# Performance work log

Hardware: AMD Instinct MI355X
Metric: run time of the kernel (lower is better)

Reference implementation:

```python
import jax, jax.numpy as jnp
import numpy as np

N = 20000       # nodes
E = 320000      # edges (before self-loops)
F_IN = 1024     # num_features
H = 4           # head_num
C = 64          # hidden_size
NC = 4          # n_classes
NEG_SLOPE = 0.2 # PyG GATConv default


def setup_inputs() -> dict:
    key = jax.random.key(0)
    ks = jax.random.split(key, 16)
    def w(k, shape, fan_in):
        return jax.random.normal(k, shape, dtype=jnp.float32) / np.sqrt(fan_in)
    x = jax.random.normal(ks[0], (N, F_IN), dtype=jnp.float32)
    edge_index = jax.random.randint(ks[1], (2, E), 0, N, dtype=jnp.int64)
    return {
        "x": x,
        "edge_index": edge_index,
        # layer 1: F_IN -> H*C, concat
        "w1": w(ks[2], (F_IN, H * C), F_IN),
        "as1": w(ks[3], (H, C), C),
        "ad1": w(ks[4], (H, C), C),
        "b1": jnp.zeros((H * C,), jnp.float32),
        # layer 2: H*C -> H*C, concat
        "w2": w(ks[5], (H * C, H * C), H * C),
        "as2": w(ks[6], (H, C), C),
        "ad2": w(ks[7], (H, C), C),
        "b2": jnp.zeros((H * C,), jnp.float32),
        # out layer: H*C -> C, 1 head, concat=False
        "w3": w(ks[8], (H * C, 1 * C), H * C),
        "as3": w(ks[9], (1, C), C),
        "ad3": w(ks[10], (1, C), C),
        "b3": jnp.zeros((C,), jnp.float32),
        # classifier
        "wc": w(ks[11], (C, NC), C),
        "bc": jnp.zeros((NC,), jnp.float32),
    }


def gat_layer(x, src, dst, W, a_src, a_dst, bias, concat):
    """PyG GATConv (eval mode, self-loops already added to src/dst)."""
    n = x.shape[0]
    Hh, Cc = a_src.shape
    h = (x @ W).reshape(n, Hh, Cc)                       # [N,H,C]
    al_s = jnp.sum(h * a_src[None], axis=-1)             # [N,H]
    al_d = jnp.sum(h * a_dst[None], axis=-1)             # [N,H]
    e = al_s[src] + al_d[dst]                            # [E,H]
    e = jax.nn.leaky_relu(e, NEG_SLOPE)
    # segment softmax over incoming edges of each destination node
    emax = jax.ops.segment_max(e, dst, num_segments=n)   # [N,H]
    ex = jnp.exp(e - emax[dst])
    denom = jax.ops.segment_sum(ex, dst, num_segments=n) # [N,H]
    alpha = ex / (denom[dst] + 1e-16)                    # [E,H]
    msg = h[src] * alpha[..., None]                      # [E,H,C]
    out = jax.ops.segment_sum(msg, dst, num_segments=n)  # [N,H,C]
    if concat:
        out = out.reshape(n, Hh * Cc)
    else:
        out = out.mean(axis=1)
    return out + bias


def reference(x, edge_index, w1, as1, ad1, b1, w2, as2, ad2, b2,
              w3, as3, ad3, b3, wc, bc):
    n = x.shape[0]
    loop = jnp.arange(n, dtype=edge_index.dtype)
    src = jnp.concatenate([edge_index[0], loop])
    dst = jnp.concatenate([edge_index[1], loop])
    out = jax.nn.relu(gat_layer(x, src, dst, w1, as1, ad1, b1, True))
    out = jax.nn.relu(gat_layer(out, src, dst, w2, as2, ad2, b2, True))
    out = gat_layer(out, src, dst, w3, as3, ad3, b3, False)
    return out @ wc + bc                                  # [N, n_classes]
```

## Files before the change

kernel.cpp:

```cpp
#include <hip/hip_runtime.h>

#define N_NODES 20000
#define N_EDGES 320000
#define ET (N_EDGES + N_NODES)
#define F_IN 1024
#define HC 256
#define NC 4

typedef unsigned short ushort_t;
typedef __attribute__((ext_vector_type(8))) short short8;
typedef __attribute__((ext_vector_type(4))) float f32x4;

__device__ inline ushort_t f2bf(float f) {
    unsigned u = __float_as_uint(f);
    unsigned r = (u + 0x7fffu + ((u >> 16) & 1u)) >> 16;
    return (ushort_t)r;
}
__device__ inline float bf2f(ushort_t u) {
    return __uint_as_float(((unsigned)u) << 16);
}

__device__ inline unsigned cvt_pk_bf16(float lo, float hi) {
    unsigned r;
    asm("v_cvt_pk_bf16_f32 %0, %1, %2" : "=v"(r) : "v"(lo), "v"(hi));
    return r;
}

#define GLOAD16(gp, lp) __builtin_amdgcn_global_load_lds( \
    (const __attribute__((address_space(1))) void*)(gp),  \
    (__attribute__((address_space(3))) void*)(lp), 16, 0, 0)

__global__ void prep_kernel(const int* __restrict__ ei, int* __restrict__ counts,
                            const float* __restrict__ w1, ushort_t* __restrict__ w1Th,
                            ushort_t* __restrict__ w1Tl,
                            const float* __restrict__ w2, ushort_t* __restrict__ w2Th,
                            ushort_t* __restrict__ w2Tl,
                            const float* __restrict__ w3, ushort_t* __restrict__ w3Th,
                            ushort_t* __restrict__ w3Tl) {
    const int EB = (ET + 255) / 256;
    const int S1 = F_IN * HC / 256;
    const int S2 = HC * HC / 256;
    int b = blockIdx.x;
    if (b < EB) {
        int e = b * 256 + threadIdx.x;
        if (e < ET) {
            int dst = (e < N_EDGES) ? ei[N_EDGES + e] : (e - N_EDGES);
            atomicAdd(&counts[dst], 1);
        }
    } else if (b < EB + S1) {
        int idx = (b - EB) * 256 + threadIdx.x;
        int k = idx / HC, n = idx - k * HC;
        float v = w1[idx];
        ushort_t h = f2bf(v);
        w1Th[(size_t)n * F_IN + k] = h;
        w1Tl[(size_t)n * F_IN + k] = f2bf(v - bf2f(h));
    } else if (b < EB + S1 + S2) {
        int idx = (b - EB - S1) * 256 + threadIdx.x;
        int k = idx / HC, n = idx - k * HC;
        float v = w2[idx];
        ushort_t h = f2bf(v);
        w2Th[(size_t)n * HC + k] = h;
        w2Tl[(size_t)n * HC + k] = f2bf(v - bf2f(h));
    } else {
        int idx = (b - EB - S1 - S2) * 256 + threadIdx.x;
        int k = idx / 64, n = idx - k * 64;
        float v = w3[idx];
        ushort_t h = f2bf(v);
        w3Th[(size_t)n * HC + k] = h;
        w3Tl[(size_t)n * HC + k] = f2bf(v - bf2f(h));
    }
}

__global__ void scan_kernel(const int* __restrict__ counts, int* __restrict__ row_ptr,
                            int* __restrict__ cursor) {
    __shared__ int sums[1024];
    int t = threadIdx.x;
    const int per = (N_NODES + 1023) / 1024;
    int b = t * per;
    int e = min(b + per, N_NODES);
    int s = 0;
    for (int i = b; i < e; ++i) s += counts[i];
    sums[t] = s;
    __syncthreads();
    for (int off = 1; off < 1024; off <<= 1) {
        int v = (t >= off) ? sums[t - off] : 0;
        __syncthreads();
        sums[t] += v;
        __syncthreads();
    }
    int run = (t == 0) ? 0 : sums[t - 1];
    for (int i = b; i < e; ++i) {
        row_ptr[i] = run;
        cursor[i]  = run;
        run += counts[i];
    }
    if (t == 0) row_ptr[N_NODES] = ET;
}

__global__ void scatter_kernel(const int* __restrict__ ei, int* __restrict__ cursor,
                               int* __restrict__ col) {
    int e = blockIdx.x * blockDim.x + threadIdx.x;
    if (e >= ET) return;
    int src, dst;
    if (e < N_EDGES) { src = ei[e]; dst = ei[N_EDGES + e]; }
    else             { src = dst = e - N_EDGES; }
    int pos = atomicAdd(&cursor[dst], 1);
    col[pos] = src;
}

#define AL_EPILOGUE()                                                              \
    {                                                                              \
        float asv[NF], adv[NF];                                                    \
        _Pragma("unroll")                                                          \
        for (int j = 0; j < NF; ++j) {                                             \
            int col = bn + wn * SN + j * 16 + (lane & 15);                         \
            asv[j] = as_w[col];                                                    \
            adv[j] = ad_w[col];                                                    \
        }                                                                          \
        float* s_as = (float*)smem;                                   \
        float* s_ad = (float*)smem + 2 * BM;                                       \
        _Pragma("unroll")                                                          \
        for (int i = 0; i < MF; ++i) {                                             \
            _Pragma("unroll")                                                      \
            for (int rr = 0; rr < 4; ++rr) {                                       \
                float ps = 0.f, pd = 0.f;                                          \
                _Pragma("unroll")                                                  \
                for (int j = 0; j < NF; ++j) {                                     \
                    ps += acc[i][j][rr] * asv[j];                                  \
                    pd += acc[i][j][rr] * adv[j];                                  \
                }                                                                  \
                _Pragma("unroll")                                                  \
                for (int o = 1; o < 16; o <<= 1) {                                 \
                    ps += __shfl_xor(ps, o, 64);                                   \
                    pd += __shfl_xor(pd, o, 64);                                   \
                }                                                                  \
                if ((lane & 15) == 0) {                                            \
                    int rl = wm * SM + i * 16 + (lane >> 4) * 4 + rr;              \
                    s_as[wn * BM + rl] = ps;                                       \
                    s_ad[wn * BM + rl] = pd;                                       \
                }                                                                  \
            }                                                                      \
        }                                                                          \
        __syncthreads();                                                           \
        if (t < BM) {                                                              \
            int row = bm + t;                                                      \
            if (row < M) {                                                         \
                int hb = bn >> 6;                                                  \
                als[row * H + hb] = s_as[t] + s_as[BM + t];                        \
                ald[row * H + hb] = s_ad[t] + s_ad[BM + t];                        \
            }                                                                      \
        }                                                                          \
    }

template<int GY>
__launch_bounds__(256)
__global__ void gemm_f32a_ks(const float* __restrict__ X,
                             const ushort_t* __restrict__ BTh, const ushort_t* __restrict__ BTl,
                             float* __restrict__ Cp0, float* __restrict__ Cp1,
                             int M, int K, int NT) {
    constexpr int BM = 128, BN = 64, SM = 64, SN = 32, MF = 4, NF = 2;
    __shared__ __align__(16) char smem[49152];

    const int t = threadIdx.x, lane = t & 63, w = t >> 6;
    const int wm = w >> 1, wn = w & 1;
    const int nwg = gridDim.x;
    const int id = blockIdx.x;
    const int q = nwg >> 3, r = nwg & 7;
    const int xcd = id & 7, idx = id >> 3;
    const int logical = (xcd < r ? xcd * (q + 1) : r * (q + 1) + (xcd - r) * q) + idx;
    const int nwg_half = nwg >> 1;
    const int ks = logical / nwg_half;
    const int rem = logical - ks * nwg_half;
    const int bm = (rem / GY) * BM, bn = (rem % GY) * BN;
    const int kbase = ks * (K >> 1);
    float* Cp = ks ? Cp1 : Cp0;

    size_t gA[4]; int lA[4];
    #pragma unroll
    for (int qq = 0; qq < 4; ++qq) {
        int row  = (w * 4 + qq) * 8 + (lane >> 3);
        int grow = min(bm + row, M - 1);
        int sw16 = ((((lane >> 1) & 3) ^ (row & 3)) << 1) | (lane & 1);
        gA[qq] = ((size_t)grow * K + kbase) * 4 + sw16 * 16;
        lA[qq] = (w * 4 + qq) * 1024;
    }
    const int gchunk = ((lane & 3) ^ ((lane >> 3) & 3)) * 16;
    const int brow = w * 16 + (lane >> 2);
    const size_t gB = (size_t)(bn + brow) * K * 2 + (size_t)kbase * 2 + gchunk;
    const int lB = w * 1024;

    const char* Xb  = (const char*)X;
    const char* Bhb = (const char*)BTh;
    const char* Blb = (const char*)BTl;
    const int c16 = (lane >> 4);
    const int NTs = K >> 7;

    f32x4 acc[MF][NF];
    #pragma unroll
    for (int i = 0; i < MF; ++i)
        #pragma unroll
        for (int j = 0; j < NF; ++j) acc[i][j] = (f32x4){0.f, 0.f, 0.f, 0.f};

    for (int ts = 0; ts < NTs; ++ts) {
        size_t kbB = (size_t)ts * 128;
        size_t kbA = (size_t)ts * 256;
        #pragma unroll
        for (int kc = 0; kc < 2; ++kc) {
            #pragma unroll
            for (int qq = 0; qq < 4; ++qq)
                GLOAD16(Xb + gA[qq] + kbA + kc * 128, smem + kc * 16384 + lA[qq]);
            GLOAD16(Bhb + gB + kbB + kc * 64, smem + 32768 + kc * 4096 + lB);
            GLOAD16(Blb + gB + kbB + kc * 64, smem + 40960 + kc * 4096 + lB);
        }
        __syncthreads();
        #pragma unroll
        for (int kc = 0; kc < 2; ++kc) {
            short8 afh[MF], afl[MF], bfh[NF], bfl[NF];
            #pragma unroll
            for (int i = 0; i < MF; ++i) {
                int row = wm * SM + i * 16 + (lane & 15);
                int off = kc * 16384 + row * 128 + ((c16 ^ (row & 3)) * 32);
                float4 a0 = *(const float4*)(smem + off);
                float4 a1 = *(const float4*)(smem + off + 16);
                unsigned h0 = cvt_pk_bf16(a0.x, a0.y);
                unsigned h1 = cvt_pk_bf16(a0.z, a0.w);
                unsigned h2 = cvt_pk_bf16(a1.x, a1.y);
                unsigned h3 = cvt_pk_bf16(a1.z, a1.w);
                unsigned l0 = cvt_pk_bf16(a0.x - __uint_as_float(h0 << 16),
                                          a0.y - __uint_as_float(h0 & 0xFFFF0000u));
                unsigned l1 = cvt_pk_bf16(a0.z - __uint_as_float(h1 << 16),
                                          a0.w - __uint_as_float(h1 & 0xFFFF0000u));
                unsigned l2 = cvt_pk_bf16(a1.x - __uint_as_float(h2 << 16),
                                          a1.y - __uint_as_float(h2 & 0xFFFF0000u));
                unsigned l3 = cvt_pk_bf16(a1.z - __uint_as_float(h3 << 16),
                                          a1.w - __uint_as_float(h3 & 0xFFFF0000u));
                uint4 hv = make_uint4(h0, h1, h2, h3);
                uint4 lv = make_uint4(l0, l1, l2, l3);
                afh[i] = *(short8*)&hv;
                afl[i] = *(short8*)&lv;
            }
            #pragma unroll
            for (int j = 0; j < NF; ++j) {
                int row = wn * SN + j * 16 + (lane & 15);
                int off = row * 64 + ((c16 ^ ((row >> 1) & 3)) * 16);
                bfh[j] = *(const short8*)(smem + 32768 + kc * 4096 + off);
                bfl[j] = *(const short8*)(smem + 40960 + kc * 4096 + off);
            }
            #pragma unroll
            for (int i = 0; i < MF; ++i)
                #pragma unroll
                for (int j = 0; j < NF; ++j) {
                    acc[i][j] = __builtin_amdgcn_mfma_f32_16x16x32_bf16(afh[i], bfh[j], acc[i][j], 0, 0, 0);
                    acc[i][j] = __builtin_amdgcn_mfma_f32_16x16x32_bf16(afh[i], bfl[j], acc[i][j], 0, 0, 0);
                    acc[i][j] = __builtin_amdgcn_mfma_f32_16x16x32_bf16(afl[i], bfh[j], acc[i][j], 0, 0, 0);
                }
        }
        __syncthreads();
    }
    #pragma unroll
    for (int i = 0; i < MF; ++i) {
        int rbase = bm + wm * SM + i * 16 + (lane >> 4) * 4;
        #pragma unroll
        for (int j = 0; j < NF; ++j) {
            int col = bn + wn * SN + j * 16 + (lane & 15);
            #pragma unroll
            for (int rr = 0; rr < 4; ++rr)
                if (rbase + rr < M) Cp[(size_t)(rbase + rr) * NT + col] = acc[i][j][rr];
        }
    }
}

__launch_bounds__(256)
__global__ void reduce_al(float* __restrict__ B0, const float* __restrict__ Cp1,
                          const float* __restrict__ as_w, const float* __restrict__ ad_w,
                          float* __restrict__ als, float* __restrict__ ald) {
    int lane = threadIdx.x & 63, w = threadIdx.x >> 6;
    int row = blockIdx.x * 4 + w;
    if (row >= N_NODES) return;
    size_t base = (size_t)row * HC + lane * 4;
    float4 p0 = *(const float4*)&B0[base];
    float4 p1 = *(const float4*)&Cp1[base];
    float4 s = make_float4(p0.x + p1.x, p0.y + p1.y, p0.z + p1.z, p0.w + p1.w);
    *(float4*)&B0[base] = s;
    int head = lane >> 4;
    int cw = (lane & 15) * 4;
    float ps = s.x * as_w[head * 64 + cw + 0] + s.y * as_w[head * 64 + cw + 1]
             + s.z * as_w[head * 64 + cw + 2] + s.w * as_w[head * 64 + cw + 3];
    float pd = s.x * ad_w[head * 64 + cw + 0] + s.y * ad_w[head * 64 + cw + 1]
             + s.z * ad_w[head * 64 + cw + 2] + s.w * ad_w[head * 64 + cw + 3];
    #pragma unroll
    for (int o = 1; o < 16; o <<= 1) {
        ps += __shfl_xor(ps, o, 64);
        pd += __shfl_xor(pd, o, 64);
    }
    if ((lane & 15) == 0) {
        als[row * 4 + head] = ps;
        ald[row * 4 + head] = pd;
    }
}

template<int BMT, int GY, int H>
__launch_bounds__(256)
__global__ void gemm_mfma(const ushort_t* __restrict__ Ah, const ushort_t* __restrict__ Al,
                          const ushort_t* __restrict__ BTh, const ushort_t* __restrict__ BTl,
                          float* __restrict__ C, const float* __restrict__ as_w,
                          const float* __restrict__ ad_w, float* __restrict__ als,
                          float* __restrict__ ald, int M, int K, int NT) {
    constexpr int BM = BMT, BN = 64, SM = BM / 2, SN = 32, MF = SM / 16, NF = 2;
    constexpr int AQ = BM / 64;
    constexpr int ASZ = BM * 64;
    __shared__ __align__(16) char smem[4 * ASZ + 16384];

    const int t = threadIdx.x, lane = t & 63, w = t >> 6;
    const int wm = w >> 1, wn = w & 1;
    const int nwg = gridDim.x;
    const int id = blockIdx.x;
    const int q = nwg >> 3, r = nwg & 7;
    const int xcd = id & 7, idx = id >> 3;
    const int logical = (xcd < r ? xcd * (q + 1) : r * (q + 1) + (xcd - r) * q) + idx;
    const int bm = (logical / GY) * BM, bn = (logical % GY) * BN;
    const int gchunk = ((lane & 3) ^ ((lane >> 3) & 3)) * 16;

    size_t gA[AQ]; int lA[AQ];
    #pragma unroll
    for (int qq = 0; qq < AQ; ++qq) {
        int inst = w * AQ + qq;
        int arow = inst * 16 + (lane >> 2);
        int grow = min(bm + arow, M - 1);
        gA[qq] = (size_t)grow * K * 2 + gchunk;
        lA[qq] = inst * 1024;
    }
    const int brow = w * 16 + (lane >> 2);
    const size_t gB = (size_t)(bn + brow) * K * 2 + gchunk;
    const int lB = w * 1024;

    const char* Ahb = (const char*)Ah;
    const char* Alb = (const char*)Al;
    const char* Bhb = (const char*)BTh;
    const char* Blb = (const char*)BTl;
    const int c16 = (lane >> 4);
    const int NTs = K / 64;

    f32x4 acc[MF][NF];
    #pragma unroll
    for (int i = 0; i < MF; ++i)
        #pragma unroll
        for (int j = 0; j < NF; ++j) acc[i][j] = (f32x4){0.f, 0.f, 0.f, 0.f};

    for (int ts = 0; ts < NTs; ++ts) {
        size_t kb = (size_t)ts * 128;
        #pragma unroll
        for (int kc = 0; kc < 2; ++kc) {
            #pragma unroll
            for (int qq = 0; qq < AQ; ++qq) {
                GLOAD16(Ahb + gA[qq] + kb + kc * 64, smem + kc * ASZ + lA[qq]);
                GLOAD16(Alb + gA[qq] + kb + kc * 64, smem + 2 * ASZ + kc * ASZ + lA[qq]);
            }
            GLOAD16(Bhb + gB + kb + kc * 64, smem + 4 * ASZ + kc * 4096 + lB);
            GLOAD16(Blb + gB + kb + kc * 64, smem + 4 * ASZ + 8192 + kc * 4096 + lB);
        }
        __syncthreads();
        #pragma unroll
        for (int kc = 0; kc < 2; ++kc) {
            short8 afh[MF], afl[MF], bfh[NF], bfl[NF];
            #pragma unroll
            for (int i = 0; i < MF; ++i) {
                int row = wm * SM + i * 16 + (lane & 15);
                int off = row * 64 + ((c16 ^ ((row >> 1) & 3)) * 16);
                afh[i] = *(const short8*)(smem + kc * ASZ + off);
                afl[i] = *(const short8*)(smem + 2 * ASZ + kc * ASZ + off);
            }
            #pragma unroll
            for (int j = 0; j < NF; ++j) {
                int row = wn * SN + j * 16 + (lane & 15);
                int off = row * 64 + ((c16 ^ ((row >> 1) & 3)) * 16);
                bfh[j] = *(const short8*)(smem + 4 * ASZ + kc * 4096 + off);
                bfl[j] = *(const short8*)(smem + 4 * ASZ + 8192 + kc * 4096 + off);
            }
            #pragma unroll
            for (int i = 0; i < MF; ++i)
                #pragma unroll
                for (int j = 0; j < NF; ++j) {
                    acc[i][j] = __builtin_amdgcn_mfma_f32_16x16x32_bf16(afh[i], bfh[j], acc[i][j], 0, 0, 0);
                    acc[i][j] = __builtin_amdgcn_mfma_f32_16x16x32_bf16(afh[i], bfl[j], acc[i][j], 0, 0, 0);
                    acc[i][j] = __builtin_amdgcn_mfma_f32_16x16x32_bf16(afl[i], bfh[j], acc[i][j], 0, 0, 0);
                }
        }
        __syncthreads();
    }
    #pragma unroll
    for (int i = 0; i < MF; ++i) {
        int rbase = bm + wm * SM + i * 16 + (lane >> 4) * 4;
        #pragma unroll
        for (int j = 0; j < NF; ++j) {
            int col = bn + wn * SN + j * 16 + (lane & 15);
            #pragma unroll
            for (int rr = 0; rr < 4; ++rr)
                if (rbase + rr < M) C[(size_t)(rbase + rr) * NT + col] = acc[i][j][rr];
        }
    }
    AL_EPILOGUE()
}

template<int CT, int CW, int H, bool RELU, bool SPLIT, bool CLS>
__launch_bounds__(256)
__global__ void agg_v6(const float* __restrict__ h, const float* __restrict__ als,
                       const float* __restrict__ ald,
                       const int* __restrict__ row_ptr, const int* __restrict__ col,
                       const float* __restrict__ bias,
                       ushort_t* __restrict__ oh, ushort_t* __restrict__ ol,
                       float* __restrict__ of,
                       const float* __restrict__ wc, const float* __restrict__ bc,
                       float* __restrict__ cls_out) {
    constexpr int NS  = CT / CW;
    constexpr int LPT = CW / 4;
    constexpr int TPW = 64 / LPT;
    static_assert(NS == H, "slice==head mapping");
    __shared__ int   s_src[4][64];
    __shared__ float s_alp[4][64];
    const int nwg = gridDim.x;
    const int q = nwg >> 3;
    int id = blockIdx.x;
    int logical = (id & 7) * q + (id >> 3);
    int slice = logical / (N_NODES / 4);
    int g = logical - slice * (N_NODES / 4);
    int lane = threadIdx.x & 63, w = threadIdx.x >> 6;
    int dst = g * 4 + w;
    int beg = row_ptr[dst], deg = row_ptr[dst + 1] - beg;
    int team = lane / LPT;
    int cc = (lane & (LPT - 1)) * 4;

    const int*   colP = col + beg;
    const float* hS   = h + slice * CW + cc;
    float ad = ald[dst * H + slice];

    float m = -1e30f, den = 0.f;
    for (int base = 0; base < deg; base += 64) {
        int i = base + lane;
        if (i < deg) {
            float e = als[colP[i] * H + slice] + ad;
            e = (e > 0.f) ? e : 0.2f * e;
            float nm = fmaxf(m, e);
            den = den * __expf(m - nm) + __expf(e - nm);
            m = nm;
        }
    }
    #pragma unroll
    for (int off = 1; off < 64; off <<= 1) {
        float mo = __shfl_xor(m, off, 64);
        float dn = __shfl_xor(den, off, 64);
        float nm = fmaxf(m, mo);
        den = den * __expf(m - nm) + dn * __expf(mo - nm);
        m = nm;
    }
    float rden = 1.f / (den + 1e-16f);

    float4 a0v = make_float4(0.f, 0.f, 0.f, 0.f);
    float4 a1v = make_float4(0.f, 0.f, 0.f, 0.f);
    float4 a2v = make_float4(0.f, 0.f, 0.f, 0.f);
    float4 a3v = make_float4(0.f, 0.f, 0.f, 0.f);
    for (int base = 0; base < deg; base += 64) {
        int cnt = min(64, deg - base);
        if (lane < cnt) {
            int src = colP[base + lane];
            s_src[w][lane] = src;
            float e = als[src * H + slice] + ad;
            e = (e > 0.f) ? e : 0.2f * e;
            s_alp[w][lane] = __expf(e - m) * rden;
        }
        int i = team;
        for (; i + 3 * TPW < cnt; i += 4 * TPW) {
            int   s0 = s_src[w][i],           s1 = s_src[w][i + TPW];
            int   s2 = s_src[w][i + 2 * TPW], s3 = s_src[w][i + 3 * TPW];
            float a0 = s_alp[w][i],           a1 = s_alp[w][i + TPW];
            float a2 = s_alp[w][i + 2 * TPW], a3 = s_alp[w][i + 3 * TPW];
            float4 h0 = *(const float4*)&hS[s0 * CT];
            float4 h1 = *(const float4*)&hS[s1 * CT];
            float4 h2 = *(const float4*)&hS[s2 * CT];
            float4 h3 = *(const float4*)&hS[s3 * CT];
            a0v.x += a0 * h0.x; a0v.y += a0 * h0.y; a0v.z += a0 * h0.z; a0v.w += a0 * h0.w;
            a1v.x += a1 * h1.x; a1v.y += a1 * h1.y; a1v.z += a1 * h1.z; a1v.w += a1 * h1.w;
            a2v.x += a2 * h2.x; a2v.y += a2 * h2.y; a2v.z += a2 * h2.z; a2v.w += a2 * h2.w;
            a3v.x += a3 * h3.x; a3v.y += a3 * h3.y; a3v.z += a3 * h3.z; a3v.w += a3 * h3.w;
        }
        for (; i < cnt; i += TPW) {
            int   s0 = s_src[w][i];
            float a0 = s_alp[w][i];
            float4 h0 = *(const float4*)&hS[s0 * CT];
            a0v.x += a0 * h0.x; a0v.y += a0 * h0.y; a0v.z += a0 * h0.z; a0v.w += a0 * h0.w;
        }
    }
    float4 acc = make_float4((a0v.x + a1v.x) + (a2v.x + a3v.x),
                             (a0v.y + a1v.y) + (a2v.y + a3v.y),
                             (a0v.z + a1v.z) + (a2v.z + a3v.z),
                             (a0v.w + a1v.w) + (a2v.w + a3v.w));
    #pragma unroll
    for (int off = LPT; off < 64; off <<= 1) {
        acc.x += __shfl_xor(acc.x, off, 64);
        acc.y += __shfl_xor(acc.y, off, 64);
        acc.z += __shfl_xor(acc.z, off, 64);
        acc.w += __shfl_xor(acc.w, off, 64);
    }
    if (team == 0) {
        int ch = slice * CW + cc;
        float4 bv = *(const float4*)&bias[ch];
        float v0 = acc.x + bv.x, v1 = acc.y + bv.y, v2 = acc.z + bv.z, v3 = acc.w + bv.w;
        if (RELU) {
            v0 = fmaxf(v0, 0.f); v1 = fmaxf(v1, 0.f);
            v2 = fmaxf(v2, 0.f); v3 = fmaxf(v3, 0.f);
        }
        if (CLS) {
            float ps[NC];
            #pragma unroll
            for (int k = 0; k < NC; ++k)
                ps[k] = v0 * wc[(cc + 0) * NC + k] + v1 * wc[(cc + 1) * NC + k]
                      + v2 * wc[(cc + 2) * NC + k] + v3 * wc[(cc + 3) * NC + k];
            #pragma unroll
            for (int o = 1; o < 16; o <<= 1)
                #pragma unroll
                for (int k = 0; k < NC; ++k) ps[k] += __shfl_xor(ps[k], o, 64);
            if (lane == 0) {
                #pragma unroll
                for (int k = 0; k < NC; ++k) cls_out[(size_t)dst * NC + k] = ps[k] + bc[k];
            }
        } else {
            size_t idx = (size_t)dst * CT + ch;
            if (SPLIT) {
                ushort4 h4, l4;
                h4.x = f2bf(v0); l4.x = f2bf(v0 - bf2f(h4.x));
                h4.y = f2bf(v1); l4.y = f2bf(v1 - bf2f(h4.y));
                h4.z = f2bf(v2); l4.z = f2bf(v2 - bf2f(h4.z));
                h4.w = f2bf(v3); l4.w = f2bf(v3 - bf2f(h4.w));
                *(ushort4*)&oh[idx] = h4;
                *(ushort4*)&ol[idx] = l4;
            } else {
                *(float4*)&of[idx] = make_float4(v0, v1, v2, v3);
            }
        }
    }
}

extern "C" void kernel_launch(void* const* d_in, const int* in_sizes, int n_in,
                              void* d_out, int out_size, void* d_ws, size_t ws_size,
                              hipStream_t stream) {
    const float* x   = (const float*)d_in[0];
    const int*   ei  = (const int*)d_in[1];
    const float* w1  = (const float*)d_in[2];
    const float* as1 = (const float*)d_in[3];
    const float* ad1 = (const float*)d_in[4];
    const float* b1  = (const float*)d_in[5];
    const float* w2  = (const float*)d_in[6];
    const float* as2 = (const float*)d_in[7];
    const float* ad2 = (const float*)d_in[8];
    const float* b2  = (const float*)d_in[9];
    const float* w3  = (const float*)d_in[10];
    const float* as3 = (const float*)d_in[11];
    const float* ad3 = (const float*)d_in[12];
    const float* b3  = (const float*)d_in[13];
    const float* wc  = (const float*)d_in[14];
    const float* bc  = (const float*)d_in[15];
    float* out = (float*)d_out;

    char* ws = (char*)d_ws;
    size_t off = 0;
    auto alloc = [&](size_t bytes) -> char* {
        char* p = ws + off;
        off = (off + bytes + 255) & ~(size_t)255;
        return p;
    };

    int* counts  = (int*)alloc(N_NODES * 4);
    int* cursor  = (int*)alloc(N_NODES * 4);
    int* row_ptr = (int*)alloc((N_NODES + 1) * 4);
    int* colidx  = (int*)alloc(ET * 4);
    float* als   = (float*)alloc(N_NODES * 4 * 4);
    float* ald   = (float*)alloc(N_NODES * 4 * 4);
    float* B0    = (float*)alloc((size_t)N_NODES * HC * 4);
    float* Cp1   = (float*)alloc((size_t)N_NODES * HC * 4);

    ushort_t* w1Th = (ushort_t*)alloc((size_t)F_IN * HC * 2);
    ushort_t* w1Tl = (ushort_t*)alloc((size_t)F_IN * HC * 2);
    ushort_t* w2Th = (ushort_t*)alloc((size_t)HC * HC * 2);
    ushort_t* w2Tl = (ushort_t*)alloc((size_t)HC * HC * 2);
    ushort_t* w3Th = (ushort_t*)alloc((size_t)HC * 64 * 2);
    ushort_t* w3Tl = (ushort_t*)alloc((size_t)HC * 64 * 2);
    ushort_t* B1h  = (ushort_t*)alloc((size_t)N_NODES * HC * 2);
    ushort_t* B1l  = (ushort_t*)alloc((size_t)N_NODES * HC * 2);

    hipMemsetAsync(counts, 0, N_NODES * sizeof(int), stream);
    const int EB = (ET + 255) / 256;
    const int PREP = EB + F_IN * HC / 256 + HC * HC / 256 + HC * 64 / 256;
    prep_kernel<<<PREP, 256, 0, stream>>>(ei, counts, w1, w1Th, w1Tl,
                                          w2, w2Th, w2Tl, w3, w3Th, w3Tl);
    scan_kernel<<<1, 1024, 0, stream>>>(counts, row_ptr, cursor);
    scatter_kernel<<<EB, 256, 0, stream>>>(ei, cursor, colidx);

    const int nwg128 = ((N_NODES + 127) / 128) * (HC / 64);
    const int nblk_dst = N_NODES / 4;
    gemm_f32a_ks<4><<<2 * nwg128, 256, 0, stream>>>(x, w1Th, w1Tl, B0, Cp1, N_NODES, F_IN, HC);
    reduce_al<<<nblk_dst, 256, 0, stream>>>(B0, Cp1, as1, ad1, als, ald);
    agg_v6<256, 64, 4, true, true, false><<<4 * nblk_dst, 256, 0, stream>>>(
        B0, als, ald, row_ptr, colidx, b1, B1h, B1l, nullptr, nullptr, nullptr, nullptr);
    gemm_mfma<128, 4, 4><<<nwg128, 256, 0, stream>>>(B1h, B1l, w2Th, w2Tl, B0, as2, ad2,
                                                     als, ald, N_NODES, HC, HC);
    agg_v6<256, 64, 4, true, true, false><<<4 * nblk_dst, 256, 0, stream>>>(
        B0, als, ald, row_ptr, colidx, b2, B1h, B1l, nullptr, nullptr, nullptr, nullptr);
    const int nwg3 = (N_NODES + 63) / 64;
    gemm_mfma<64, 1, 1><<<nwg3, 256, 0, stream>>>(B1h, B1l, w3Th, w3Tl, B0, as3, ad3,
                                                  als, ald, N_NODES, HC, 64);
    agg_v6<64, 64, 1, false, false, true><<<nblk_dst, 256, 0, stream>>>(
        B0, als, ald, row_ptr, colidx, b3, nullptr, nullptr, nullptr, wc, bc, out);
}
```

Before: 287.6 us.

## Load A operand directly from global into registers, bypassing LDS staging

The fp32 X tile is now read straight from global memory into registers, laid out to match the MFMA fragments, and no longer staged through shared memory with swizzled writes and reads. LDS use shrinks from 48KB to 16KB, which may allow more resident workgroups, and one LDS round trip per tile is gone. In exchange, the A reads lose LDS-side coalescing and reuse: the two waves sharing the same rows now each fetch them from global or L2, so redundant global traffic and register pressure both rise.

After: 321.2 us. +11.7%, slower.

```diff
diff --git a/kernel.cpp b/kernel.cpp
--- a/kernel.cpp
+++ b/kernel.cpp
@@ -159,7 +159,7 @@
                              float* __restrict__ Cp0, float* __restrict__ Cp1,
                              int M, int K, int NT) {
     constexpr int BM = 128, BN = 64, SM = 64, SN = 32, MF = 4, NF = 2;
-    __shared__ __align__(16) char smem[49152];
+    __shared__ __align__(16) char smem[16384];
 
     const int t = threadIdx.x, lane = t & 63, w = t >> 6;
     const int wm = w >> 1, wn = w & 1;
@@ -175,21 +175,17 @@
     const int kbase = ks * (K >> 1);
     float* Cp = ks ? Cp1 : Cp0;
 
-    size_t gA[4]; int lA[4];
-    #pragma unroll
-    for (int qq = 0; qq < 4; ++qq) {
-        int row  = (w * 4 + qq) * 8 + (lane >> 3);
-        int grow = min(bm + row, M - 1);
-        int sw16 = ((((lane >> 1) & 3) ^ (row & 3)) << 1) | (lane & 1);
-        gA[qq] = ((size_t)grow * K + kbase) * 4 + sw16 * 16;
-        lA[qq] = (w * 4 + qq) * 1024;
+    const float* aPtr[MF];
+    #pragma unroll
+    for (int i = 0; i < MF; ++i) {
+        int row = min(bm + wm * SM + i * 16 + (lane & 15), M - 1);
+        aPtr[i] = X + (size_t)row * K + kbase + (lane >> 4) * 8;
     }
     const int gchunk = ((lane & 3) ^ ((lane >> 3) & 3)) * 16;
     const int brow = w * 16 + (lane >> 2);
     const size_t gB = (size_t)(bn + brow) * K * 2 + (size_t)kbase * 2 + gchunk;
     const int lB = w * 1024;
 
-    const char* Xb  = (const char*)X;
     const char* Bhb = (const char*)BTh;
     const char* Blb = (const char*)BTl;
     const int c16 = (lane >> 4);
@@ -202,15 +198,20 @@
         for (int j = 0; j < NF; ++j) acc[i][j] = (f32x4){0.f, 0.f, 0.f, 0.f};
 
     for (int ts = 0; ts < NTs; ++ts) {
+        int ko = ts * 64;
+        float4 cA[MF][2][2];
+        #pragma unroll
+        for (int i = 0; i < MF; ++i)
+            #pragma unroll
+            for (int kc = 0; kc < 2; ++kc) {
+                cA[i][kc][0] = *(const float4*)(aPtr[i] + ko + kc * 32);
+                cA[i][kc][1] = *(const float4*)(aPtr[i] + ko + kc * 32 + 4);
+            }
         size_t kbB = (size_t)ts * 128;
-        size_t kbA = (size_t)ts * 256;
         #pragma unroll
         for (int kc = 0; kc < 2; ++kc) {
-            #pragma unroll
-            for (int qq = 0; qq < 4; ++qq)
-                GLOAD16(Xb + gA[qq] + kbA + kc * 128, smem + kc * 16384 + lA[qq]);
-            GLOAD16(Bhb + gB + kbB + kc * 64, smem + 32768 + kc * 4096 + lB);
-            GLOAD16(Blb + gB + kbB + kc * 64, smem + 40960 + kc * 4096 + lB);
+            GLOAD16(Bhb + gB + kbB + kc * 64, smem + kc * 4096 + lB);
+            GLOAD16(Blb + gB + kbB + kc * 64, smem + 8192 + kc * 4096 + lB);
         }
         __syncthreads();
         #pragma unroll
@@ -218,10 +219,7 @@
             short8 afh[MF], afl[MF], bfh[NF], bfl[NF];
             #pragma unroll
             for (int i = 0; i < MF; ++i) {
-                int row = wm * SM + i * 16 + (lane & 15);
-                int off = kc * 16384 + row * 128 + ((c16 ^ (row & 3)) * 32);
-                float4 a0 = *(const float4*)(smem + off);
-                float4 a1 = *(const float4*)(smem + off + 16);
+                float4 a0 = cA[i][kc][0], a1 = cA[i][kc][1];
                 unsigned h0 = cvt_pk_bf16(a0.x, a0.y);
                 unsigned h1 = cvt_pk_bf16(a0.z, a0.w);
                 unsigned h2 = cvt_pk_bf16(a1.x, a1.y);
@@ -243,8 +241,8 @@
             for (int j = 0; j < NF; ++j) {
                 int row = wn * SN + j * 16 + (lane & 15);
                 int off = row * 64 + ((c16 ^ ((row >> 1) & 3)) * 16);
-                bfh[j] = *(const short8*)(smem + 32768 + kc * 4096 + off);
-                bfl[j] = *(const short8*)(smem + 40960 + kc * 4096 + off);
+                bfh[j] = *(const short8*)(smem + kc * 4096 + off);
+                bfl[j] = *(const short8*)(smem + 8192 + kc * 4096 + off);
             }
             #pragma unroll
             for (int i = 0; i < MF; ++i)
```
